# Kernel optimization log

Hardware: AMD Instinct MI355X
Metric: run time of the kernel (lower is better)

## Reference

```python
import jax, jax.numpy as jnp
import numpy as np

D_MODEL = 1024
NUM_HEADS = 16
HEAD_DIM = D_MODEL // NUM_HEADS  # 64
D_FF = 4096
EPS = 1e-5


def layer_norm(x, gamma, beta):
    mu = jnp.mean(x, axis=-1, keepdims=True)
    var = jnp.mean((x - mu) ** 2, axis=-1, keepdims=True)
    return (x - mu) * jax.lax.rsqrt(var + EPS) * gamma + beta


def apply_rope(t):
    # t: [B, H, S, head_dim]; interleaved-pair rotation as in RoPE.apply_rope
    S, d = t.shape[-2], t.shape[-1]
    inv_freq = 1.0 / (10000.0 ** (jnp.arange(0, d, 2, dtype=jnp.float32) / d))  # [d/2]
    angles = jnp.arange(S, dtype=jnp.float32)[:, None] * inv_freq[None, :]      # [S, d/2]
    sin, cos = jnp.sin(angles), jnp.cos(angles)
    tp = t.reshape(*t.shape[:-1], d // 2, 2)  # pairs of adjacent elements
    t0, t1 = tp[..., 0], tp[..., 1]
    rot = jnp.stack([t0 * cos - t1 * sin, t0 * sin + t1 * cos], axis=-1)
    return rot.reshape(t.shape)


def setup_inputs() -> dict:
    key = jax.random.key(0)
    ks = jax.random.split(key, 18)
    s = 0.02
    d, f = D_MODEL, D_FF
    return {
        "x": jax.random.normal(ks[0], (2, 2048, d), dtype=jnp.float32),
        "Wq": jax.random.normal(ks[1], (d, d), dtype=jnp.float32) * s,
        "bq": jnp.zeros((d,), jnp.float32),
        "Wk": jax.random.normal(ks[2], (d, d), dtype=jnp.float32) * s,
        "bk": jnp.zeros((d,), jnp.float32),
        "Wv": jax.random.normal(ks[3], (d, d), dtype=jnp.float32) * s,
        "bv": jnp.zeros((d,), jnp.float32),
        "Wo": jax.random.normal(ks[4], (d, d), dtype=jnp.float32) * s,
        "bo": jnp.zeros((d,), jnp.float32),
        "W1": jax.random.normal(ks[5], (d, f), dtype=jnp.float32) * s,
        "b1": jnp.zeros((f,), jnp.float32),
        "W2": jax.random.normal(ks[6], (f, d), dtype=jnp.float32) * s,
        "b2": jnp.zeros((d,), jnp.float32),
        "g1": jnp.ones((d,), jnp.float32),
        "beta1": jnp.zeros((d,), jnp.float32),
        "g2": jnp.ones((d,), jnp.float32),
        "beta2": jnp.zeros((d,), jnp.float32),
    }


def reference(x, Wq, bq, Wk, bk, Wv, bv, Wo, bo, W1, b1, W2, b2, g1, beta1, g2, beta2):
    B, S, d = x.shape
    H, hd = NUM_HEADS, HEAD_DIM
    x_norm = layer_norm(x, g1, beta1)
    q = (x_norm @ Wq + bq).reshape(B, S, H, hd).transpose(0, 2, 1, 3)  # [B,H,S,hd]
    k = (x_norm @ Wk + bk).reshape(B, S, H, hd).transpose(0, 2, 1, 3)
    v = (x_norm @ Wv + bv).reshape(B, S, H, hd).transpose(0, 2, 1, 3)
    q = apply_rope(q)
    k = apply_rope(k)
    q = q * (1.0 / jnp.sqrt(jnp.float32(hd)))
    scores = jnp.einsum("bhqd,bhkd->bhqk", q, k)  # [B,H,S,S]
    attn = jax.nn.softmax(scores, axis=-1)
    out = jnp.einsum("bhqk,bhkd->bhqd", attn, v)
    out = out.transpose(0, 2, 1, 3).reshape(B, S, d)
    attn_out = out @ Wo + bo
    x = x + attn_out  # dropout p=0 (eval)
    x_norm2 = layer_norm(x, g2, beta2)
    ffn = jax.nn.relu(x_norm2 @ W1 + b1) @ W2 + b2
    return x + ffn
```

## Files before the change

### kernel.cpp

```cpp
#include <hip/hip_runtime.h>

typedef unsigned short bf16_t;
typedef short short8 __attribute__((ext_vector_type(8)));
typedef float f32x4 __attribute__((ext_vector_type(4)));

static __device__ __forceinline__ unsigned short f2bf(float f) {
  unsigned int u = __float_as_uint(f);
  unsigned int r = (u + 0x7FFFu + ((u >> 16) & 1u)) >> 16;
  return (unsigned short)r;
}
static __device__ __forceinline__ unsigned short f2bf_fast(float f) {
  return (unsigned short)((__float_as_uint(f) + 0x8000u) >> 16);
}
static __device__ __forceinline__ float bf2f(unsigned short u) {
  return __uint_as_float((unsigned int)u << 16);
}

__device__ __forceinline__ void gload_lds16(const void* g, void* l) {
  __builtin_amdgcn_global_load_lds((const __attribute__((address_space(1))) void*)g,
                                   (__attribute__((address_space(3))) void*)l,
                                   16, 0, 0);
}

__global__ __launch_bounds__(256) void prep_kernel(
    const float* __restrict__ Wq, const float* __restrict__ Wk,
    const float* __restrict__ Wv, const float* __restrict__ Wo,
    const float* __restrict__ W1, const float* __restrict__ W2,
    const float* __restrict__ x, const float* __restrict__ g1,
    const float* __restrict__ be1,
    bf16_t* __restrict__ WqkvT, bf16_t* __restrict__ W1T,
    bf16_t* __restrict__ W2T, bf16_t* __restrict__ xnb) {
  __shared__ float tile[32][33];
  const int bid = blockIdx.x;
  if (bid < 12288) {
    const float* src;
    bf16_t* dst;
    int rows, cols, bx, by;
    if (bid < 4096) {
      const int z = bid >> 10, r = bid & 1023;
      src = (z == 0) ? Wq : (z == 1) ? Wk : (z == 2) ? Wv : Wo;
      dst = WqkvT + (size_t)z * 1048576;
      rows = 1024; cols = 1024;
      bx = (r & 31) * 32; by = (r >> 5) * 32;
    } else if (bid < 8192) {
      const int r = bid - 4096;
      src = W1; dst = W1T; rows = 1024; cols = 4096;
      bx = (r & 127) * 32; by = (r >> 7) * 32;
    } else {
      const int r = bid - 8192;
      src = W2; dst = W2T; rows = 4096; cols = 1024;
      bx = (r & 31) * 32; by = (r >> 5) * 32;
    }
    const int tx = threadIdx.x & 31, ty = threadIdx.x >> 5;
#pragma unroll
    for (int i = 0; i < 32; i += 8)
      tile[ty + i][tx] = src[(size_t)(by + ty + i) * cols + (bx + tx)];
    __syncthreads();
#pragma unroll
    for (int i = 0; i < 32; i += 8)
      dst[(size_t)(bx + ty + i) * rows + (by + tx)] = f2bf(tile[tx][ty + i]);
  } else {
    const int row = bid - 12288;
    const int tid = threadIdx.x;
    const float4 v = reinterpret_cast<const float4*>(x + (size_t)row * 1024)[tid];
    float s = v.x + v.y + v.z + v.w;
    float ss = v.x * v.x + v.y * v.y + v.z * v.z + v.w * v.w;
#pragma unroll
    for (int off = 32; off; off >>= 1) {
      s += __shfl_xor(s, off, 64);
      ss += __shfl_xor(ss, off, 64);
    }
    float* red = &tile[0][0];
    const int wave = tid >> 6, lane = tid & 63;
    if (lane == 0) { red[wave] = s; red[4 + wave] = ss; }
    __syncthreads();
    const float mu = (red[0] + red[1] + red[2] + red[3]) * (1.f / 1024.f);
    const float ms = (red[4] + red[5] + red[6] + red[7]) * (1.f / 1024.f);
    const float rstd = rsqrtf(ms - mu * mu + 1e-5f);
    const float4 gg = reinterpret_cast<const float4*>(g1)[tid];
    const float4 bb = reinterpret_cast<const float4*>(be1)[tid];
    bf16_t* o = xnb + (size_t)row * 1024 + tid * 4;
    o[0] = f2bf((v.x - mu) * rstd * gg.x + bb.x);
    o[1] = f2bf((v.y - mu) * rstd * gg.y + bb.y);
    o[2] = f2bf((v.z - mu) * rstd * gg.z + bb.z);
    o[3] = f2bf((v.w - mu) * rstd * gg.w + bb.w);
  }
}

__global__ __launch_bounds__(256) void ln2_combine(const bf16_t* __restrict__ p,
                                                   const float* __restrict__ x,
                                                   const float* __restrict__ bo,
                                                   const float* __restrict__ g,
                                                   const float* __restrict__ be,
                                                   float* __restrict__ x2,
                                                   bf16_t* __restrict__ xn) {
  const int row = blockIdx.x;
  const int tid = threadIdx.x;
  const float4 xv = reinterpret_cast<const float4*>(x + (size_t)row * 1024)[tid];
  const float4 bb = reinterpret_cast<const float4*>(bo)[tid];
  float4 v = {bb.x + xv.x, bb.y + xv.y, bb.z + xv.z, bb.w + xv.w};
#pragma unroll
  for (int z = 0; z < 4; ++z) {
    const ushort4 a = reinterpret_cast<const ushort4*>(p + (size_t)z * 4194304 + (size_t)row * 1024)[tid];
    v.x += bf2f(a.x); v.y += bf2f(a.y); v.z += bf2f(a.z); v.w += bf2f(a.w);
  }
  reinterpret_cast<float4*>(x2 + (size_t)row * 1024)[tid] = v;
  float s = v.x + v.y + v.z + v.w;
  float ss = v.x * v.x + v.y * v.y + v.z * v.z + v.w * v.w;
#pragma unroll
  for (int off = 32; off; off >>= 1) {
    s += __shfl_xor(s, off, 64);
    ss += __shfl_xor(ss, off, 64);
  }
  __shared__ float red[8];
  const int wave = tid >> 6, lane = tid & 63;
  if (lane == 0) { red[wave] = s; red[4 + wave] = ss; }
  __syncthreads();
  const float mu = (red[0] + red[1] + red[2] + red[3]) * (1.f / 1024.f);
  const float ms = (red[4] + red[5] + red[6] + red[7]) * (1.f / 1024.f);
  const float rstd = rsqrtf(ms - mu * mu + 1e-5f);
  const float4 gg = reinterpret_cast<const float4*>(g)[tid];
  const float4 eb = reinterpret_cast<const float4*>(be)[tid];
  bf16_t* o = xn + (size_t)row * 1024 + tid * 4;
  o[0] = f2bf((v.x - mu) * rstd * gg.x + eb.x);
  o[1] = f2bf((v.y - mu) * rstd * gg.y + eb.y);
  o[2] = f2bf((v.z - mu) * rstd * gg.z + eb.z);
  o[3] = f2bf((v.w - mu) * rstd * gg.w + eb.w);
}

__global__ __launch_bounds__(256) void ffn_combine(const bf16_t* __restrict__ p0,
                                                   const bf16_t* __restrict__ p2,
                                                   const float* __restrict__ x2,
                                                   const float* __restrict__ b2,
                                                   float* __restrict__ out) {
  const int row = blockIdx.x;
  const int tid = threadIdx.x;
  const ushort4 a0 = reinterpret_cast<const ushort4*>(p0 + (size_t)row * 1024)[tid];
  const ushort4 a1 = reinterpret_cast<const ushort4*>(p0 + 4194304 + (size_t)row * 1024)[tid];
  const ushort4 a2 = reinterpret_cast<const ushort4*>(p2 + (size_t)row * 1024)[tid];
  const float4 xv = reinterpret_cast<const float4*>(x2 + (size_t)row * 1024)[tid];
  const float4 bb = reinterpret_cast<const float4*>(b2)[tid];
  float4 v;
  v.x = bf2f(a0.x) + bf2f(a1.x) + bf2f(a2.x) + bb.x + xv.x;
  v.y = bf2f(a0.y) + bf2f(a1.y) + bf2f(a2.y) + bb.y + xv.y;
  v.z = bf2f(a0.z) + bf2f(a1.z) + bf2f(a2.z) + bb.z + xv.z;
  v.w = bf2f(a0.w) + bf2f(a1.w) + bf2f(a2.w) + bb.w + xv.w;
  reinterpret_cast<float4*>(out + (size_t)row * 1024)[tid] = v;
}

__global__ __launch_bounds__(256) void rope_bf16(bf16_t* __restrict__ q,
                                                 bf16_t* __restrict__ k) {
  const int id = blockIdx.x * 256 + threadIdx.x;
  const int i = id & 31;
  const int s = (id >> 5) & 2047;
  const int bh = id >> 16;
  const float inv = exp2f((float)i * -0.41524101186f);
  float sn, cs;
  sincosf((float)s * inv, &sn, &cs);
  const size_t base = ((size_t)bh * 2048 + s) * 64 + 2 * i;
  unsigned int qp = *(unsigned int*)&q[base];
  unsigned int kp = *(unsigned int*)&k[base];
  const float q0 = bf2f(qp & 0xffff), q1 = bf2f(qp >> 16);
  const float k0 = bf2f(kp & 0xffff), k1 = bf2f(kp >> 16);
  const float qs = 0.18033688f;
  const unsigned int qo =
      (unsigned int)f2bf((q0 * cs - q1 * sn) * qs) |
      ((unsigned int)f2bf((q0 * sn + q1 * cs) * qs) << 16);
  const unsigned int ko =
      (unsigned int)f2bf(k0 * cs - k1 * sn) |
      ((unsigned int)f2bf(k0 * sn + k1 * cs) << 16);
  *(unsigned int*)&q[base] = qo;
  *(unsigned int*)&k[base] = ko;
}

__global__ __launch_bounds__(256) void vtrans(const bf16_t* __restrict__ v,
                                              bf16_t* __restrict__ vt) {
  __shared__ bf16_t tile[32][33];
  const int bh = blockIdx.x;
  const int s0 = blockIdx.y * 32;
  const int d0 = blockIdx.z * 32;
  const int tx = threadIdx.x & 31, ty = threadIdx.x >> 5;
  const size_t base = (size_t)bh * (2048 * 64);
#pragma unroll
  for (int i = 0; i < 32; i += 8)
    tile[ty + i][tx] = v[base + (size_t)(s0 + ty + i) * 64 + d0 + tx];
  __syncthreads();
#pragma unroll
  for (int i = 0; i < 32; i += 8)
    vt[base + (size_t)(d0 + ty + i) * 2048 + s0 + tx] = tile[tx][ty + i];
}

__global__ __launch_bounds__(256) void attn3(const bf16_t* __restrict__ qb,
                                             const bf16_t* __restrict__ kb,
                                             const bf16_t* __restrict__ vt,
                                             bf16_t* __restrict__ out) {
  const int bh = blockIdx.x;
  const int tid = threadIdx.x, wave = tid >> 6, lane = tid & 63;
  const int col = lane & 15, quad = lane >> 4;
  const int q0 = blockIdx.y * 128 + wave * 32;
  const size_t kvb = (size_t)bh * (2048 * 64);

  __shared__ __align__(16) bf16_t Ks[4096];
  __shared__ __align__(16) bf16_t Vs[4096];
  __shared__ __align__(16) bf16_t psw_all[4 * 32 * 72];
  bf16_t* psw = psw_all + wave * (32 * 72);

  short8 qf[2][2];
#pragma unroll
  for (int mi = 0; mi < 2; ++mi)
#pragma unroll
    for (int ks = 0; ks < 2; ++ks)
      qf[mi][ks] = *(const short8*)&qb[kvb + (size_t)(q0 + mi * 16 + col) * 64 + ks * 32 + quad * 8];

  f32x4 acc[2][4];
  float lsum[2][4];
#pragma unroll
  for (int mi = 0; mi < 2; ++mi)
#pragma unroll
    for (int n = 0; n < 4; ++n) acc[mi][n] = (f32x4){0.f, 0.f, 0.f, 0.f};
#pragma unroll
  for (int mi = 0; mi < 2; ++mi)
#pragma unroll
    for (int r = 0; r < 4; ++r) lsum[mi][r] = 0.f;

  const int swz = (col & 7);

  for (int t = 0; t < 2048; t += 64) {
#pragma unroll
    for (int j = 0; j < 2; ++j) {
      const int s = wave * 128 + j * 64 + lane;
      const int r = s >> 3;
      const int c = (s & 7) ^ (r & 7);
      gload_lds16(kb + kvb + (size_t)(t + r) * 64 + c * 8, Ks + (size_t)(wave * 128 + j * 64) * 8);
      gload_lds16(vt + kvb + (size_t)r * 2048 + t + c * 8, Vs + (size_t)(wave * 128 + j * 64) * 8);
    }
    __syncthreads();
    f32x4 sc[2][4];
#pragma unroll
    for (int mi = 0; mi < 2; ++mi)
#pragma unroll
      for (int n = 0; n < 4; ++n) sc[mi][n] = (f32x4){0.f, 0.f, 0.f, 0.f};
#pragma unroll
    for (int ks = 0; ks < 2; ++ks) {
      short8 kf[4];
#pragma unroll
      for (int n = 0; n < 4; ++n) {
        const int R = n * 16 + col;
        const int C = (ks * 4 + quad) ^ swz;
        kf[n] = *(const short8*)&Ks[(size_t)(R * 8 + C) * 8];
      }
#pragma unroll
      for (int mi = 0; mi < 2; ++mi)
#pragma unroll
        for (int n = 0; n < 4; ++n)
          sc[mi][n] = __builtin_amdgcn_mfma_f32_16x16x32_bf16(qf[mi][ks], kf[n], sc[mi][n], 0, 0, 0);
    }
#pragma unroll
    for (int mi = 0; mi < 2; ++mi)
#pragma unroll
      for (int n = 0; n < 4; ++n)
#pragma unroll
        for (int r = 0; r < 4; ++r) {
          const float pv = exp2f(sc[mi][n][r]);
          lsum[mi][r] += pv;
          psw[(mi * 16 + quad * 4 + r) * 72 + n * 16 + col] = f2bf_fast(pv);
        }
    short8 pf[2][2];
#pragma unroll
    for (int mi = 0; mi < 2; ++mi)
#pragma unroll
      for (int ks = 0; ks < 2; ++ks)
        pf[mi][ks] = *(const short8*)&psw[(mi * 16 + col) * 72 + ks * 32 + quad * 8];
#pragma unroll
    for (int ks = 0; ks < 2; ++ks) {
      short8 vf[4];
#pragma unroll
      for (int n = 0; n < 4; ++n) {
        const int R = n * 16 + col;
        const int C = (ks * 4 + quad) ^ swz;
        vf[n] = *(const short8*)&Vs[(size_t)(R * 8 + C) * 8];
      }
#pragma unroll
      for (int mi = 0; mi < 2; ++mi)
#pragma unroll
        for (int n = 0; n < 4; ++n)
          acc[mi][n] = __builtin_amdgcn_mfma_f32_16x16x32_bf16(pf[mi][ks], vf[n], acc[mi][n], 0, 0, 0);
    }
    __syncthreads();
  }

  const int b = bh >> 4, h = bh & 15;
#pragma unroll
  for (int mi = 0; mi < 2; ++mi)
#pragma unroll
    for (int r = 0; r < 4; ++r) {
      float s = lsum[mi][r];
      s += __shfl_xor(s, 1, 64);
      s += __shfl_xor(s, 2, 64);
      s += __shfl_xor(s, 4, 64);
      s += __shfl_xor(s, 8, 64);
      const float rl = 1.f / s;
      const size_t ro = (size_t)(b * 2048 + q0 + mi * 16 + quad * 4 + r) * 1024 + h * 64;
#pragma unroll
      for (int n = 0; n < 4; ++n) out[ro + n * 16 + col] = f2bf(acc[mi][n][r] * rl);
    }
}

enum { MODE_QKV = 0, MODE_FF1 = 1, MODE_PART = 2 };

template <int MODE>
__global__ __launch_bounds__(256) void gemm_bt(
    const bf16_t* __restrict__ A, const bf16_t* __restrict__ BT,
    int M, int N, int K, int kspan,
    const float* __restrict__ bias0, const float* __restrict__ bias1,
    const float* __restrict__ bias2,
    bf16_t* __restrict__ ob0, bf16_t* __restrict__ ob1, bf16_t* __restrict__ ob2) {
  __shared__ __align__(16) char smem[34816];
  bf16_t* As = (bf16_t*)smem;
  bf16_t* Bs = (bf16_t*)(smem + 16384);
  const int tid = threadIdx.x;
  const int wave = tid >> 6, lane = tid & 63;
  const int row16 = lane & 15, quad = lane >> 4;
  const int m0 = blockIdx.x * 128, n0 = blockIdx.y * 128;
  const int wm = (wave & 1) << 6, wn = (wave >> 1) << 6;

  f32x4 acc[4][4];
#pragma unroll
  for (int i = 0; i < 4; ++i)
#pragma unroll
    for (int j = 0; j < 4; ++j) acc[i][j] = (f32x4){0.f, 0.f, 0.f, 0.f};

  const int kb = blockIdx.z * kspan;
  const int kend = (kb + kspan < K) ? kb + kspan : K;

  for (int k0 = kb; k0 < kend; k0 += 64) {
#pragma unroll
    for (int j = 0; j < 4; ++j) {
      const int s = j * 256 + tid;
      const int r = s >> 3;
      const int cg = ((s & 7) ^ (r & 7)) << 3;
      gload_lds16(A + (size_t)(m0 + r) * K + k0 + cg, As + (size_t)s * 8);
      gload_lds16(BT + (size_t)(n0 + r) * K + k0 + cg, Bs + (size_t)s * 8);
    }
    __syncthreads();
    const int sw = row16 & 7;
#pragma unroll
    for (int kk = 0; kk < 2; ++kk) {
      short8 af[4], bfr[4];
#pragma unroll
      for (int mi = 0; mi < 4; ++mi)
        af[mi] = *(const short8*)&As[(size_t)(wm + mi * 16 + row16) * 64 + (((kk << 2) | quad) ^ sw) * 8];
#pragma unroll
      for (int ni = 0; ni < 4; ++ni)
        bfr[ni] = *(const short8*)&Bs[(size_t)(wn + ni * 16 + row16) * 64 + (((kk << 2) | quad) ^ sw) * 8];
#pragma unroll
      for (int mi = 0; mi < 4; ++mi)
#pragma unroll
        for (int ni = 0; ni < 4; ++ni)
          acc[mi][ni] =
              __builtin_amdgcn_mfma_f32_16x16x32_bf16(af[mi], bfr[ni], acc[mi][ni], 0, 0, 0);
    }
    __syncthreads();
  }

  bf16_t* ct = (bf16_t*)smem;
#pragma unroll
  for (int mi = 0; mi < 4; ++mi)
#pragma unroll
    for (int ni = 0; ni < 4; ++ni) {
      const int gn = n0 + wn + ni * 16 + row16;
      float bsv = 0.f;
      if (MODE == MODE_QKV)
        bsv = (gn < 1024) ? bias0[gn] : (gn < 2048) ? bias1[gn - 1024] : bias2[gn - 2048];
      else if (MODE == MODE_FF1)
        bsv = bias0[gn];
#pragma unroll
      for (int r = 0; r < 4; ++r) {
        float c = acc[mi][ni][r] + bsv;
        if (MODE == MODE_FF1) c = fmaxf(c, 0.f);
        ct[(size_t)(wm + mi * 16 + quad * 4 + r) * 136 + wn + ni * 16 + row16] = f2bf(c);
      }
    }
  __syncthreads();
  const int lr0 = tid >> 4, lc = tid & 15;
#pragma unroll
  for (int i = 0; i < 8; ++i) {
    const int lr = i * 16 + lr0;
    const uint4 v = *(const uint4*)&ct[(size_t)lr * 136 + lc * 8];
    const int gm = m0 + lr;
    if (MODE == MODE_QKV) {
      const int nn = (n0 & 1023) + lc * 8;
      const int h = nn >> 6, d = nn & 63;
      const int b = gm >> 11, s = gm & 2047;
      bf16_t* dst = (n0 < 1024) ? ob0 : (n0 < 2048) ? ob1 : ob2;
      *(uint4*)&dst[(((size_t)b * 16 + h) * 2048 + s) * 64 + d] = v;
    } else if (MODE == MODE_FF1) {
      *(uint4*)&ob0[(size_t)gm * N + n0 + lc * 8] = v;
    } else {
      bf16_t* dst = (blockIdx.z == 2) ? ob1 : ob0 + (size_t)blockIdx.z * 4194304;
      *(uint4*)&dst[(size_t)gm * N + n0 + lc * 8] = v;
    }
  }
}

extern "C" void kernel_launch(void* const* d_in, const int* in_sizes, int n_in,
                              void* d_out, int out_size, void* d_ws, size_t ws_size,
                              hipStream_t stream) {
  const float* x = (const float*)d_in[0];
  const float* Wq = (const float*)d_in[1];
  const float* bq = (const float*)d_in[2];
  const float* Wk = (const float*)d_in[3];
  const float* bk = (const float*)d_in[4];
  const float* Wv = (const float*)d_in[5];
  const float* bv = (const float*)d_in[6];
  const float* Wo = (const float*)d_in[7];
  const float* bo = (const float*)d_in[8];
  const float* W1 = (const float*)d_in[9];
  const float* b1 = (const float*)d_in[10];
  const float* W2 = (const float*)d_in[11];
  const float* b2 = (const float*)d_in[12];
  const float* g1 = (const float*)d_in[13];
  const float* be1 = (const float*)d_in[14];
  const float* g2 = (const float*)d_in[15];
  const float* be2 = (const float*)d_in[16];
  float* out = (float*)d_out;

  char* ws = (char*)d_ws;
  size_t off = 0;
  auto alloc = [&](size_t bytes) {
    void* p = ws + off;
    off += (bytes + 255) & ~(size_t)255;
    return p;
  };
  bf16_t* WqkvT = (bf16_t*)alloc(3072ULL * 1024 * 2);
  bf16_t* WoT = (bf16_t*)alloc(1024ULL * 1024 * 2);
  bf16_t* W1T = (bf16_t*)alloc(4096ULL * 1024 * 2);
  bf16_t* W2T = (bf16_t*)alloc(1024ULL * 4096 * 2);
  bf16_t* xnb = (bf16_t*)alloc(4096ULL * 1024 * 2);
  bf16_t* qb = (bf16_t*)alloc(4194304ULL * 2);
  bf16_t* kb = (bf16_t*)alloc(4194304ULL * 2);
  bf16_t* vraw = (bf16_t*)alloc(4194304ULL * 2);
  bf16_t* vt = (bf16_t*)alloc(4194304ULL * 2);
  bf16_t* h1 = qb;
  bf16_t* x2p = qb;
  bf16_t* ffp = WqkvT;
  float* x2 = (float*)alloc(16777216ULL);

  prep_kernel<<<16384, 256, 0, stream>>>(Wq, Wk, Wv, Wo, W1, W2, x, g1, be1,
                                         WqkvT, W1T, W2T, xnb);

  gemm_bt<MODE_QKV><<<dim3(32, 24, 1), 256, 0, stream>>>(xnb, WqkvT, 4096, 3072, 1024, 1024,
                                                         bq, bk, bv, qb, kb, vraw);

  rope_bf16<<<8192, 256, 0, stream>>>(qb, kb);

  vtrans<<<dim3(32, 64, 2), 256, 0, stream>>>(vraw, vt);

  attn3<<<dim3(32, 16), 256, 0, stream>>>(qb, kb, vt, xnb);

  gemm_bt<MODE_PART><<<dim3(32, 8, 4), 256, 0, stream>>>(xnb, WoT, 4096, 1024, 1024, 256,
                                                         nullptr, nullptr, nullptr,
                                                         x2p, x2p + 2 * 4194304, nullptr);

  ln2_combine<<<4096, 256, 0, stream>>>(x2p, x, bo, g2, be2, x2, xnb);

  gemm_bt<MODE_FF1><<<dim3(32, 32, 1), 256, 0, stream>>>(xnb, W1T, 4096, 4096, 1024, 1024,
                                                         b1, nullptr, nullptr,
                                                         h1, nullptr, nullptr);

  gemm_bt<MODE_PART><<<dim3(32, 8, 3), 256, 0, stream>>>(h1, W2T, 4096, 1024, 4096, 1408,
                                                         nullptr, nullptr, nullptr,
                                                         ffp, xnb, nullptr);

  ffn_combine<<<4096, 256, 0, stream>>>(ffp, xnb, x2, b2, out);
}
```

Before: 380.8 us.

## Rewrite attention with 32x32 MFMA, register-resident P and double-buffered K/V

The attention kernel now uses 32x32x16 bf16 MFMAs and computes S^T = K·Q, so the P tile already sits in registers in the layout the PV MFMA expects. It is packed with v_cvt_pk_bf16 and v_permlane32_swap instead of being round-tripped through LDS. K/V tiles are double-buffered so the next tile's global->LDS loads overlap compute, which drops one barrier per iteration. This removes LDS traffic and sync, at the cost of more LDS for the buffers and reliance on gfx950-specific instructions.

```diff
diff --git a/kernel.cpp b/kernel.cpp
--- a/kernel.cpp
+++ b/kernel.cpp
@@ -3,17 +3,24 @@
 typedef unsigned short bf16_t;
 typedef short short8 __attribute__((ext_vector_type(8)));
 typedef float f32x4 __attribute__((ext_vector_type(4)));
+typedef float f32x16 __attribute__((ext_vector_type(16)));
+typedef unsigned int u32x4 __attribute__((ext_vector_type(4)));
 
 static __device__ __forceinline__ unsigned short f2bf(float f) {
   unsigned int u = __float_as_uint(f);
   unsigned int r = (u + 0x7FFFu + ((u >> 16) & 1u)) >> 16;
   return (unsigned short)r;
 }
-static __device__ __forceinline__ unsigned short f2bf_fast(float f) {
-  return (unsigned short)((__float_as_uint(f) + 0x8000u) >> 16);
-}
 static __device__ __forceinline__ float bf2f(unsigned short u) {
   return __uint_as_float((unsigned int)u << 16);
+}
+static __device__ __forceinline__ unsigned int cvt_pk_bf16(float lo, float hi) {
+  unsigned int r;
+  asm("v_cvt_pk_bf16_f32 %0, %1, %2" : "=v"(r) : "v"(lo), "v"(hi));
+  return r;
+}
+static __device__ __forceinline__ void pl32swap(unsigned int& a, unsigned int& b) {
+  asm("v_permlane32_swap_b32 %0, %1" : "+v"(a), "+v"(b));
 }
 
 __device__ __forceinline__ void gload_lds16(const void* g, void* l) {
@@ -190,120 +197,119 @@
     vt[base + (size_t)(d0 + ty + i) * 2048 + s0 + tx] = tile[tx][ty + i];
 }
 
-__global__ __launch_bounds__(256) void attn3(const bf16_t* __restrict__ qb,
+__global__ __launch_bounds__(256) void attn4(const bf16_t* __restrict__ qb,
                                              const bf16_t* __restrict__ kb,
                                              const bf16_t* __restrict__ vt,
                                              bf16_t* __restrict__ out) {
   const int bh = blockIdx.x;
   const int tid = threadIdx.x, wave = tid >> 6, lane = tid & 63;
-  const int col = lane & 15, quad = lane >> 4;
+  const int l31 = lane & 31, hi = lane >> 5;
   const int q0 = blockIdx.y * 128 + wave * 32;
   const size_t kvb = (size_t)bh * (2048 * 64);
 
-  __shared__ __align__(16) bf16_t Ks[4096];
-  __shared__ __align__(16) bf16_t Vs[4096];
-  __shared__ __align__(16) bf16_t psw_all[4 * 32 * 72];
-  bf16_t* psw = psw_all + wave * (32 * 72);
-
-  short8 qf[2][2];
-#pragma unroll
-  for (int mi = 0; mi < 2; ++mi)
-#pragma unroll
-    for (int ks = 0; ks < 2; ++ks)
-      qf[mi][ks] = *(const short8*)&qb[kvb + (size_t)(q0 + mi * 16 + col) * 64 + ks * 32 + quad * 8];
-
-  f32x4 acc[2][4];
-  float lsum[2][4];
-#pragma unroll
-  for (int mi = 0; mi < 2; ++mi)
-#pragma unroll
-    for (int n = 0; n < 4; ++n) acc[mi][n] = (f32x4){0.f, 0.f, 0.f, 0.f};
-#pragma unroll
-  for (int mi = 0; mi < 2; ++mi)
-#pragma unroll
-    for (int r = 0; r < 4; ++r) lsum[mi][r] = 0.f;
-
-  const int swz = (col & 7);
+  __shared__ __align__(16) bf16_t Ks[2][4096];
+  __shared__ __align__(16) bf16_t Vs[2][4096];
+  __shared__ float lred[4][32];
+
+  short8 qf[4];
+#pragma unroll
+  for (int st = 0; st < 4; ++st)
+    qf[st] = *(const short8*)&qb[kvb + (size_t)(q0 + l31) * 64 + st * 16 + hi * 8];
+
+  f32x16 acc0, acc1;
+#pragma unroll
+  for (int r = 0; r < 16; ++r) { acc0[r] = 0.f; acc1[r] = 0.f; }
+  float ls0 = 0.f, ls1 = 0.f, ls2 = 0.f, ls3 = 0.f;
+
+#pragma unroll
+  for (int j = 0; j < 2; ++j) {
+    const int s = wave * 128 + j * 64 + lane;
+    const int r = s >> 3;
+    const int c = (s & 7) ^ (r & 7);
+    gload_lds16(kb + kvb + (size_t)r * 64 + c * 8, &Ks[0][(size_t)s * 8]);
+    gload_lds16(vt + kvb + (size_t)r * 2048 + c * 8, &Vs[0][(size_t)s * 8]);
+  }
+  __syncthreads();
 
   for (int t = 0; t < 2048; t += 64) {
-#pragma unroll
-    for (int j = 0; j < 2; ++j) {
-      const int s = wave * 128 + j * 64 + lane;
-      const int r = s >> 3;
-      const int c = (s & 7) ^ (r & 7);
-      gload_lds16(kb + kvb + (size_t)(t + r) * 64 + c * 8, Ks + (size_t)(wave * 128 + j * 64) * 8);
-      gload_lds16(vt + kvb + (size_t)r * 2048 + t + c * 8, Vs + (size_t)(wave * 128 + j * 64) * 8);
+    const int cur = (t >> 6) & 1;
+    if (t + 64 < 2048) {
+#pragma unroll
+      for (int j = 0; j < 2; ++j) {
+        const int s = wave * 128 + j * 64 + lane;
+        const int r = s >> 3;
+        const int c = (s & 7) ^ (r & 7);
+        gload_lds16(kb + kvb + (size_t)(t + 64 + r) * 64 + c * 8, &Ks[cur ^ 1][(size_t)s * 8]);
+        gload_lds16(vt + kvb + (size_t)r * 2048 + (t + 64) + c * 8, &Vs[cur ^ 1][(size_t)s * 8]);
+      }
+    }
+    f32x16 p0, p1;
+#pragma unroll
+    for (int r = 0; r < 16; ++r) { p0[r] = 0.f; p1[r] = 0.f; }
+#pragma unroll
+    for (int st = 0; st < 4; ++st) {
+      const int R0 = l31, R1 = 32 + l31;
+      const short8 kf0 = *(const short8*)&Ks[cur][(size_t)(R0 * 8 + (((st << 1) | hi) ^ (R0 & 7))) * 8];
+      const short8 kf1 = *(const short8*)&Ks[cur][(size_t)(R1 * 8 + (((st << 1) | hi) ^ (R1 & 7))) * 8];
+      p0 = __builtin_amdgcn_mfma_f32_32x32x16_bf16(kf0, qf[st], p0, 0, 0, 0);
+      p1 = __builtin_amdgcn_mfma_f32_32x32x16_bf16(kf1, qf[st], p1, 0, 0, 0);
+    }
+#pragma unroll
+    for (int f = 0; f < 2; ++f) {
+      f32x16& p = f ? p1 : p0;
+      float e[16];
+#pragma unroll
+      for (int r = 0; r < 16; ++r) e[r] = exp2f(p[r]);
+      ls0 += e[0] + e[1] + e[2] + e[3];
+      ls1 += e[4] + e[5] + e[6] + e[7];
+      ls2 += e[8] + e[9] + e[10] + e[11];
+      ls3 += e[12] + e[13] + e[14] + e[15];
+      unsigned int a0 = cvt_pk_bf16(e[0], e[1]), b0 = cvt_pk_bf16(e[4], e[5]);
+      unsigned int a1 = cvt_pk_bf16(e[2], e[3]), b1 = cvt_pk_bf16(e[6], e[7]);
+      unsigned int a2 = cvt_pk_bf16(e[8], e[9]), b2 = cvt_pk_bf16(e[12], e[13]);
+      unsigned int a3 = cvt_pk_bf16(e[10], e[11]), b3 = cvt_pk_bf16(e[14], e[15]);
+      pl32swap(a0, b0);
+      pl32swap(a1, b1);
+      pl32swap(a2, b2);
+      pl32swap(a3, b3);
+      const u32x4 w0 = {a0, a1, b0, b1};
+      const u32x4 w1 = {a2, a3, b2, b3};
+      const short8 pf0 = __builtin_bit_cast(short8, w0);
+      const short8 pf1 = __builtin_bit_cast(short8, w1);
+#pragma unroll
+      for (int ks = 0; ks < 2; ++ks) {
+        const short8 pf = ks ? pf1 : pf0;
+        {
+          const int R = l31;
+          const int C = (((f << 2) | (ks << 1) | hi) ^ (R & 7));
+          const short8 vf = *(const short8*)&Vs[cur][(size_t)(R * 8 + C) * 8];
+          acc0 = __builtin_amdgcn_mfma_f32_32x32x16_bf16(pf, vf, acc0, 0, 0, 0);
+        }
+        {
+          const int R = 32 + l31;
+          const int C = (((f << 2) | (ks << 1) | hi) ^ (R & 7));
+          const short8 vf = *(const short8*)&Vs[cur][(size_t)(R * 8 + C) * 8];
+          acc1 = __builtin_amdgcn_mfma_f32_32x32x16_bf16(pf, vf, acc1, 0, 0, 0);
+        }
+      }
     }
     __syncthreads();
-    f32x4 sc[2][4];
-#pragma unroll
-    for (int mi = 0; mi < 2; ++mi)
-#pragma unroll
-      for (int n = 0; n < 4; ++n) sc[mi][n] = (f32x4){0.f, 0.f, 0.f, 0.f};
-#pragma unroll
-    for (int ks = 0; ks < 2; ++ks) {
-      short8 kf[4];
-#pragma unroll
-      for (int n = 0; n < 4; ++n) {
-        const int R = n * 16 + col;
-        const int C = (ks * 4 + quad) ^ swz;
-        kf[n] = *(const short8*)&Ks[(size_t)(R * 8 + C) * 8];
-      }
-#pragma unroll
-      for (int mi = 0; mi < 2; ++mi)
-#pragma unroll
-        for (int n = 0; n < 4; ++n)
-          sc[mi][n] = __builtin_amdgcn_mfma_f32_16x16x32_bf16(qf[mi][ks], kf[n], sc[mi][n], 0, 0, 0);
-    }
-#pragma unroll
-    for (int mi = 0; mi < 2; ++mi)
-#pragma unroll
-      for (int n = 0; n < 4; ++n)
-#pragma unroll
-        for (int r = 0; r < 4; ++r) {
-          const float pv = exp2f(sc[mi][n][r]);
-          lsum[mi][r] += pv;
-          psw[(mi * 16 + quad * 4 + r) * 72 + n * 16 + col] = f2bf_fast(pv);
-        }
-    short8 pf[2][2];
-#pragma unroll
-    for (int mi = 0; mi < 2; ++mi)
-#pragma unroll
-      for (int ks = 0; ks < 2; ++ks)
-        pf[mi][ks] = *(const short8*)&psw[(mi * 16 + col) * 72 + ks * 32 + quad * 8];
-#pragma unroll
-    for (int ks = 0; ks < 2; ++ks) {
-      short8 vf[4];
-#pragma unroll
-      for (int n = 0; n < 4; ++n) {
-        const int R = n * 16 + col;
-        const int C = (ks * 4 + quad) ^ swz;
-        vf[n] = *(const short8*)&Vs[(size_t)(R * 8 + C) * 8];
-      }
-#pragma unroll
-      for (int mi = 0; mi < 2; ++mi)
-#pragma unroll
-        for (int n = 0; n < 4; ++n)
-          acc[mi][n] = __builtin_amdgcn_mfma_f32_16x16x32_bf16(pf[mi][ks], vf[n], acc[mi][n], 0, 0, 0);
-    }
-    __syncthreads();
-  }
+  }
+
+  float lsum = (ls0 + ls1) + (ls2 + ls3);
+  lsum += __shfl_xor(lsum, 32, 64);
+  if (lane < 32) lred[wave][l31] = lsum;
+  __syncthreads();
 
   const int b = bh >> 4, h = bh & 15;
 #pragma unroll
-  for (int mi = 0; mi < 2; ++mi)
-#pragma unroll
-    for (int r = 0; r < 4; ++r) {
-      float s = lsum[mi][r];
-      s += __shfl_xor(s, 1, 64);
-      s += __shfl_xor(s, 2, 64);
-      s += __shfl_xor(s, 4, 64);
-      s += __shfl_xor(s, 8, 64);
-      const float rl = 1.f / s;
-      const size_t ro = (size_t)(b * 2048 + q0 + mi * 16 + quad * 4 + r) * 1024 + h * 64;
-#pragma unroll
-      for (int n = 0; n < 4; ++n) out[ro + n * 16 + col] = f2bf(acc[mi][n][r] * rl);
-    }
+  for (int r = 0; r < 16; ++r) {
+    const int qrow = (r & 3) + 8 * (r >> 2) + 4 * hi;
+    const float rl = 1.f / lred[wave][qrow];
+    const size_t ro = (size_t)(b * 2048 + q0 + qrow) * 1024 + h * 64;
+    out[ro + l31] = f2bf(acc0[r] * rl);
+    out[ro + 32 + l31] = f2bf(acc1[r] * rl);
+  }
 }
 
 enum { MODE_QKV = 0, MODE_FF1 = 1, MODE_PART = 2 };
@@ -456,7 +462,7 @@
 
   vtrans<<<dim3(32, 64, 2), 256, 0, stream>>>(vraw, vt);
 
-  attn3<<<dim3(32, 16), 256, 0, stream>>>(qb, kb, vt, xnb);
+  attn4<<<dim3(32, 16), 256, 0, stream>>>(qb, kb, vt, xnb);
 
   gemm_bt<MODE_PART><<<dim3(32, 8, 4), 256, 0, stream>>>(xnb, WoT, 4096, 1024, 1024, 256,
                                                          nullptr, nullptr, nullptr,
```

After: 374.1 us. No clear change (-1.8%).
